# Optimization experiments

Hardware: AMD Instinct MI355X
Metric: run time of the kernel (lower is better)

## Reference

```python
import jax, jax.numpy as jnp
import numpy as np

N_NODES = 100000
N_EDGES = 400000
N_GRAPHS = 5000
IN, H, OUT = 11, 256, 1


def setup_inputs() -> dict:
    key = jax.random.key(0)
    ks = jax.random.split(key, 16)

    def xav(k, shape):
        fan_in, fan_out = shape[-2], shape[-1]
        std = float(np.sqrt(2.0 / (fan_in + fan_out)))
        return jax.random.normal(k, shape, dtype=jnp.float32) * std

    x = jax.random.normal(ks[0], (N_NODES, IN), dtype=jnp.float32)
    edge_index = jax.random.randint(ks[1], (2, N_EDGES), 0, N_NODES, dtype=jnp.int64)
    batch = jnp.sort(jax.random.randint(ks[2], (N_NODES,), 0, N_GRAPHS, dtype=jnp.int64))
    return {
        "x": x,
        "edge_index": edge_index,
        "batch": batch,
        "gin0_w1": xav(ks[3], (IN, H)),
        "gin0_b1": jnp.zeros((H,), jnp.float32),
        "gin0_w2": xav(ks[4], (H, H)),
        "gin0_b2": jnp.zeros((H,), jnp.float32),
        "gin_w1": xav(ks[5], (4, H, H)),
        "gin_b1": jnp.zeros((4, H), jnp.float32),
        "gin_w2": xav(ks[6], (4, H, H)),
        "gin_b2": jnp.zeros((4, H), jnp.float32),
        "head_w1": xav(ks[7], (H, H)),
        "head_b1": jnp.zeros((H,), jnp.float32),
        "head_w2": xav(ks[8], (H, OUT)),
        "head_b2": jnp.zeros((OUT,), jnp.float32),
    }


def _gin(x, src, dst, w1, b1, w2, b2):
    # GINConv (eps=0): MLP(x + sum_{j->i} x_j), then outer ReLU from forward()
    agg = jax.ops.segment_sum(x[src], dst, num_segments=N_NODES)
    h = x + agg
    h = jnp.matmul(jax.nn.relu(jnp.matmul(h, w1) + b1), w2) + b2
    return jax.nn.relu(h)  # dropout p=0.15 is identity in eval


def reference(x, edge_index, batch, gin0_w1, gin0_b1, gin0_w2, gin0_b2,
              gin_w1, gin_b1, gin_w2, gin_b2,
              head_w1, head_b1, head_w2, head_b2):
    src, dst = edge_index[0], edge_index[1]
    h = _gin(x, src, dst, gin0_w1, gin0_b1, gin0_w2, gin0_b2)
    for i in range(4):
        h = _gin(h, src, dst, gin_w1[i], gin_b1[i], gin_w2[i], gin_b2[i])
    # global mean pool over graphs
    sums = jax.ops.segment_sum(h, batch, num_segments=N_GRAPHS)
    cnts = jax.ops.segment_sum(jnp.ones((h.shape[0],), h.dtype), batch, num_segments=N_GRAPHS)
    pooled = sums / jnp.maximum(cnts, 1.0)[:, None]
    # head: Linear -> Dropout(0.25, identity in eval) -> Linear
    out = jnp.matmul(pooled, head_w1) + head_b1
    out = jnp.matmul(out, head_w2) + head_b2
    return out
```

## Files before the change

### kernel.cpp

```cpp
#include <hip/hip_runtime.h>
#include <hip/hip_bf16.h>


constexpr int HDIM = 256;

typedef short v8s __attribute__((ext_vector_type(8)));
typedef float v4f __attribute__((ext_vector_type(4)));

__device__ __forceinline__ float bflo(unsigned int u) { return __uint_as_float(u << 16); }
__device__ __forceinline__ float bfhi(unsigned int u) { return __uint_as_float(u & 0xffff0000u); }
__device__ __forceinline__ unsigned short f2bf(float f) {
    unsigned int u = __float_as_uint(f);
    return (unsigned short)((u + 0x7fffu + ((u >> 16) & 1u)) >> 16);
}

__device__ __forceinline__ void gload16(const void* g, void* l) {
    __builtin_amdgcn_global_load_lds(
        (const __attribute__((address_space(1))) unsigned int*)g,
        (__attribute__((address_space(3))) unsigned int*)l, 16, 0, 0);
}

__global__ __launch_bounds__(256) void hist_kernel(
    const int* __restrict__ dst, int* __restrict__ deg, int n_edges)
{
    int e = blockIdx.x * 256 + threadIdx.x;
    if (e < n_edges) atomicAdd(&deg[dst[e]], 1);
}

__global__ __launch_bounds__(256) void scan1_kernel(
    const int* __restrict__ deg, int* __restrict__ scanex,
    int* __restrict__ partials, int n)
{
    __shared__ int s[256];
    int i = blockIdx.x * 256 + threadIdx.x;
    int v = (i < n) ? deg[i] : 0;
    s[threadIdx.x] = v;
    __syncthreads();
#pragma unroll
    for (int off = 1; off < 256; off <<= 1) {
        int t = (threadIdx.x >= off) ? s[threadIdx.x - off] : 0;
        __syncthreads();
        s[threadIdx.x] += t;
        __syncthreads();
    }
    if (i < n) scanex[i] = s[threadIdx.x] - v;
    if (threadIdx.x == 255) partials[blockIdx.x] = s[255];
}

__global__ __launch_bounds__(512) void scan2_kernel(int* __restrict__ partials, int nb)
{
    __shared__ int s[512];
    int v = (threadIdx.x < nb) ? partials[threadIdx.x] : 0;
    s[threadIdx.x] = v;
    __syncthreads();
#pragma unroll
    for (int off = 1; off < 512; off <<= 1) {
        int t = (threadIdx.x >= off) ? s[threadIdx.x - off] : 0;
        __syncthreads();
        s[threadIdx.x] += t;
        __syncthreads();
    }
    if (threadIdx.x < nb) partials[threadIdx.x] = s[threadIdx.x] - v;
}

__global__ __launch_bounds__(256) void scan3_kernel(
    const int* __restrict__ scanex, const int* __restrict__ partials,
    int* __restrict__ rowptr, int* __restrict__ cursor, int n, int n_edges)
{
    int i = blockIdx.x * 256 + threadIdx.x;
    if (i < n) {
        int v = scanex[i] + partials[blockIdx.x];
        rowptr[i] = v;
        cursor[i] = v;
    }
    if (i == 0) rowptr[n] = n_edges;
}

__global__ __launch_bounds__(256) void fill_kernel(
    const int* __restrict__ src, const int* __restrict__ dst,
    int* __restrict__ cursor, int* __restrict__ csr_src, int n_edges)
{
    int e = blockIdx.x * 256 + threadIdx.x;
    if (e >= n_edges) return;
    int slot = atomicAdd(&cursor[dst[e]], 1);
    csr_src[slot] = src[e];
}

__global__ __launch_bounds__(256) void convw_kernel(
    const float* __restrict__ g0w2, const float* __restrict__ gw1,
    const float* __restrict__ gw2, unsigned short* __restrict__ Bts)
{
    int gid = blockIdx.x * 256 + threadIdx.x;
    if (gid >= 9 * 65536) return;
    int m = gid >> 16;
    int e = gid & 0xffff;
    int n = e >> 8, k = e & 255;
    const float* W = (m == 0) ? g0w2
                   : (m <= 4) ? gw1 + (size_t)(m - 1) * 65536
                              : gw2 + (size_t)(m - 5) * 65536;
    Bts[(size_t)m * 65536 + n * 256 + k] = f2bf(W[k * 256 + n]);
}

__global__ __launch_bounds__(256) void agg0_kernel(
    const float* __restrict__ x, const int* __restrict__ rowptr,
    const int* __restrict__ csr_src, float* __restrict__ xsum, int n)
{
    int gid = blockIdx.x * 256 + threadIdx.x;
    int node = gid >> 4, f = gid & 15;
    if (node >= n || f >= 11) return;
    float acc = x[(size_t)node * 11 + f];
    int beg = rowptr[node], end = rowptr[node + 1];
    for (int e = beg; e < end; e++)
        acc += x[(size_t)csr_src[e] * 11 + f];
    xsum[(size_t)node * 11 + f] = acc;
}

__global__ __launch_bounds__(256) void agg_bf_kernel(
    const unsigned short* __restrict__ h, const int* __restrict__ rowptr,
    const int* __restrict__ csr_src, unsigned short* __restrict__ out, int n)
{
    int node = blockIdx.x * 8 + (threadIdx.x >> 5);
    if (node >= n) return;
    int l = threadIdx.x & 31;
    uint4 raw = *(const uint4*)&h[(size_t)node * HDIM + l * 8];
    float a0 = bflo(raw.x), a1 = bfhi(raw.x), a2 = bflo(raw.y), a3 = bfhi(raw.y);
    float a4 = bflo(raw.z), a5 = bfhi(raw.z), a6 = bflo(raw.w), a7 = bfhi(raw.w);
    int beg = rowptr[node], end = rowptr[node + 1];
    for (int e = beg; e < end; e++) {
        int s = csr_src[e];
        uint4 r = *(const uint4*)&h[(size_t)s * HDIM + l * 8];
        a0 += bflo(r.x); a1 += bfhi(r.x); a2 += bflo(r.y); a3 += bfhi(r.y);
        a4 += bflo(r.z); a5 += bfhi(r.z); a6 += bflo(r.w); a7 += bfhi(r.w);
    }
    uint4 o;
    o.x = (unsigned int)f2bf(a0) | ((unsigned int)f2bf(a1) << 16);
    o.y = (unsigned int)f2bf(a2) | ((unsigned int)f2bf(a3) << 16);
    o.z = (unsigned int)f2bf(a4) | ((unsigned int)f2bf(a5) << 16);
    o.w = (unsigned int)f2bf(a6) | ((unsigned int)f2bf(a7) << 16);
    *(uint4*)&out[(size_t)node * HDIM + l * 8] = o;
}

__global__ __launch_bounds__(256) void gemm0_kernel(
    const float* __restrict__ xsum, const float* __restrict__ w1,
    const float* __restrict__ b1, unsigned short* __restrict__ out, int M)
{
    int row = blockIdx.x * 4 + (threadIdx.x >> 6);
    if (row >= M) return;
    int lane = threadIdx.x & 63;
    float xr[11];
#pragma unroll
    for (int k = 0; k < 11; k++) xr[k] = xsum[(size_t)row * 11 + k];
    int n = lane * 4;
    float4 acc = *(const float4*)&b1[n];
#pragma unroll
    for (int k = 0; k < 11; k++) {
        float4 w = *(const float4*)&w1[k * HDIM + n];
        acc.x = fmaf(xr[k], w.x, acc.x);
        acc.y = fmaf(xr[k], w.y, acc.y);
        acc.z = fmaf(xr[k], w.z, acc.z);
        acc.w = fmaf(xr[k], w.w, acc.w);
    }
    uint2 o;
    o.x = (unsigned int)f2bf(fmaxf(acc.x, 0.f)) | ((unsigned int)f2bf(fmaxf(acc.y, 0.f)) << 16);
    o.y = (unsigned int)f2bf(fmaxf(acc.z, 0.f)) | ((unsigned int)f2bf(fmaxf(acc.w, 0.f)) << 16);
    *(uint2*)&out[(size_t)row * HDIM + n] = o;
}

__global__ __launch_bounds__(256) void gemm_mfma(
    const unsigned short* __restrict__ A, const unsigned short* __restrict__ Wt,
    const float* __restrict__ bias, unsigned short* __restrict__ C,
    int M, int do_relu)
{
    __shared__ short lds[2][512 * 8];
    const int tid = threadIdx.x;
    const int w = tid >> 6, lane = tid & 63;
    const int q = lane >> 4, r = lane & 15;
    const int rh = w & 1, ch = w >> 1;
    const int m0 = blockIdx.x * 128, n0 = blockIdx.y * 128;

    v4f acc[4][4];
#pragma unroll
    for (int i = 0; i < 4; i++)
#pragma unroll
        for (int j = 0; j < 4; j++)
            acc[i][j] = (v4f){0.f, 0.f, 0.f, 0.f};

    for (int kt = 0; kt < HDIM; kt += 32) {
#pragma unroll
        for (int rd = 0; rd < 2; rd++) {
            int cb = rd * 256 + w * 64;
            int s  = cb + lane;
            int row = s >> 2;
            int ko  = ((s & 3) - (row >> 1)) & 3;
            int gr = m0 + row; if (gr >= M) gr = M - 1;
            gload16(&A[(size_t)gr * HDIM + kt + ko * 8],  &lds[0][cb * 8]);
            gload16(&Wt[(size_t)(n0 + row) * HDIM + kt + ko * 8], &lds[1][cb * 8]);
        }
        __syncthreads();
        v8s af[4], bf[4];
#pragma unroll
        for (int mi = 0; mi < 4; mi++) {
            int row = rh * 64 + mi * 16 + r;
            int slot = row * 4 + ((q + (row >> 1)) & 3);
            af[mi] = *(const v8s*)&lds[0][slot * 8];
        }
#pragma unroll
        for (int ni = 0; ni < 4; ni++) {
            int row = ch * 64 + ni * 16 + r;
            int slot = row * 4 + ((q + (row >> 1)) & 3);
            bf[ni] = *(const v8s*)&lds[1][slot * 8];
        }
#pragma unroll
        for (int mi = 0; mi < 4; mi++)
#pragma unroll
            for (int ni = 0; ni < 4; ni++)
                acc[mi][ni] = __builtin_amdgcn_mfma_f32_16x16x32_bf16(
                    af[mi], bf[ni], acc[mi][ni], 0, 0, 0);
        __syncthreads();
    }

    float bv[4];
#pragma unroll
    for (int ni = 0; ni < 4; ni++)
        bv[ni] = bias[n0 + ch * 64 + ni * 16 + r];

    short* cw = &lds[0][0] + w * (16 * 72);
#pragma unroll
    for (int mi = 0; mi < 4; mi++) {
#pragma unroll
        for (int ni = 0; ni < 4; ni++)
#pragma unroll
            for (int i = 0; i < 4; i++) {
                float v = acc[mi][ni][i] + bv[ni];
                if (do_relu) v = fmaxf(v, 0.f);
                cw[(q * 4 + i) * 72 + ni * 16 + r] = (short)f2bf(v);
            }
        __syncthreads();
        int row = lane >> 2, seg = lane & 3;
        int gm = m0 + rh * 64 + mi * 16 + row;
        if (gm < M) {
            v8s p0 = *(const v8s*)&cw[row * 72 + seg * 16];
            v8s p1 = *(const v8s*)&cw[row * 72 + seg * 16 + 8];
            size_t o = (size_t)gm * HDIM + n0 + ch * 64 + seg * 16;
            *(v8s*)&C[o]     = p0;
            *(v8s*)&C[o + 8] = p1;
        }
        __syncthreads();
    }
}

__global__ __launch_bounds__(256) void mlp_fused(
    const unsigned short* __restrict__ A,
    const unsigned short* __restrict__ W1t, const float* __restrict__ b1,
    const unsigned short* __restrict__ W2t, const float* __restrict__ b2,
    unsigned short* __restrict__ C, int M)
{
    __shared__ short Ybuf[8 * 2048];
    __shared__ short Astage[256 * 8];
    __shared__ short Wstage[1024 * 8];
    const int tid = threadIdx.x;
    const int w = tid >> 6, lane = tid & 63;
    const int q = lane >> 4, r = lane & 15;
    const int m0 = blockIdx.x * 64;

    v4f acc[4][4];
#pragma unroll
    for (int i = 0; i < 4; i++)
#pragma unroll
        for (int j = 0; j < 4; j++)
            acc[i][j] = (v4f){0.f, 0.f, 0.f, 0.f};

    for (int kc = 0; kc < 8; kc++) {
        int kt = kc * 32;
        {
            int s = tid;
            int row = s >> 2;
            int ko = ((s & 3) - (row >> 1)) & 3;
            int gr = m0 + row; if (gr >= M) gr = M - 1;
            gload16(&A[(size_t)gr * HDIM + kt + ko * 8], &Astage[(w * 64) * 8]);
        }
#pragma unroll
        for (int rd = 0; rd < 4; rd++) {
            int cb = rd * 256 + w * 64;
            int s = cb + lane;
            int n = s >> 2;
            int ko = ((s & 3) - (n >> 1)) & 3;
            gload16(&W1t[(size_t)n * HDIM + kt + ko * 8], &Wstage[cb * 8]);
        }
        __syncthreads();
        v8s af[4], bf[4];
#pragma unroll
        for (int mi = 0; mi < 4; mi++) {
            int row = mi * 16 + r;
            int slot = row * 4 + ((q + (row >> 1)) & 3);
            af[mi] = *(const v8s*)&Astage[slot * 8];
        }
#pragma unroll
        for (int ni = 0; ni < 4; ni++) {
            int n = w * 64 + ni * 16 + r;
            int slot = n * 4 + ((q + (n >> 1)) & 3);
            bf[ni] = *(const v8s*)&Wstage[slot * 8];
        }
#pragma unroll
        for (int mi = 0; mi < 4; mi++)
#pragma unroll
            for (int ni = 0; ni < 4; ni++)
                acc[mi][ni] = __builtin_amdgcn_mfma_f32_16x16x32_bf16(
                    af[mi], bf[ni], acc[mi][ni], 0, 0, 0);
        __syncthreads();
    }

    {
        float bv1[4];
#pragma unroll
        for (int ni = 0; ni < 4; ni++)
            bv1[ni] = b1[w * 64 + ni * 16 + r];
#pragma unroll
        for (int mi = 0; mi < 4; mi++)
#pragma unroll
            for (int ni = 0; ni < 4; ni++)
#pragma unroll
                for (int i = 0; i < 4; i++) {
                    float v = fmaxf(acc[mi][ni][i] + bv1[ni], 0.f);
                    int row = mi * 16 + q * 4 + i;
                    int col = w * 64 + ni * 16 + r;
                    int chunk = col >> 5, kk = col & 31;
                    int ko = kk >> 3, j = kk & 7;
                    int slot = row * 4 + ((ko + (row >> 1)) & 3);
                    Ybuf[chunk * 2048 + slot * 8 + j] = (short)f2bf(v);
                }
    }
    __syncthreads();

    v4f acc2[4][4];
#pragma unroll
    for (int i = 0; i < 4; i++)
#pragma unroll
        for (int j = 0; j < 4; j++)
            acc2[i][j] = (v4f){0.f, 0.f, 0.f, 0.f};

    for (int kc = 0; kc < 8; kc++) {
        int kt = kc * 32;
#pragma unroll
        for (int rd = 0; rd < 4; rd++) {
            int cb = rd * 256 + w * 64;
            int s = cb + lane;
            int n = s >> 2;
            int ko = ((s & 3) - (n >> 1)) & 3;
            gload16(&W2t[(size_t)n * HDIM + kt + ko * 8], &Wstage[cb * 8]);
        }
        __syncthreads();
        v8s af[4], bf[4];
#pragma unroll
        for (int mi = 0; mi < 4; mi++) {
            int row = mi * 16 + r;
            int slot = row * 4 + ((q + (row >> 1)) & 3);
            af[mi] = *(const v8s*)&Ybuf[kc * 2048 + slot * 8];
        }
#pragma unroll
        for (int ni = 0; ni < 4; ni++) {
            int n = w * 64 + ni * 16 + r;
            int slot = n * 4 + ((q + (n >> 1)) & 3);
            bf[ni] = *(const v8s*)&Wstage[slot * 8];
        }
#pragma unroll
        for (int mi = 0; mi < 4; mi++)
#pragma unroll
            for (int ni = 0; ni < 4; ni++)
                acc2[mi][ni] = __builtin_amdgcn_mfma_f32_16x16x32_bf16(
                    af[mi], bf[ni], acc2[mi][ni], 0, 0, 0);
        __syncthreads();
    }

    float bv2[4];
#pragma unroll
    for (int ni = 0; ni < 4; ni++)
        bv2[ni] = b2[w * 64 + ni * 16 + r];
    short* cw = &Ybuf[w * 1152];
#pragma unroll
    for (int mi = 0; mi < 4; mi++) {
#pragma unroll
        for (int ni = 0; ni < 4; ni++)
#pragma unroll
            for (int i = 0; i < 4; i++) {
                float v = fmaxf(acc2[mi][ni][i] + bv2[ni], 0.f);
                cw[(q * 4 + i) * 72 + ni * 16 + r] = (short)f2bf(v);
            }
        __syncthreads();
        int row = lane >> 2, seg = lane & 3;
        int gm = m0 + mi * 16 + row;
        if (gm < M) {
            v8s p0 = *(const v8s*)&cw[row * 72 + seg * 16];
            v8s p1 = *(const v8s*)&cw[row * 72 + seg * 16 + 8];
            size_t o = (size_t)gm * HDIM + w * 64 + seg * 16;
            *(v8s*)&C[o]     = p0;
            *(v8s*)&C[o + 8] = p1;
        }
        __syncthreads();
    }
}

__global__ __launch_bounds__(256) void gemm_head(
    const float* __restrict__ A, const float* __restrict__ B,
    const float* __restrict__ bias, float* __restrict__ C, int M)
{
    __shared__ float As[16][132];
    __shared__ float Bs[16][132];
    const int tid = threadIdx.x;
    const int tx = tid & 15, ty = tid >> 4;
    const int m0 = blockIdx.x * 128, n0 = blockIdx.y * 128;
    const int arow = tid >> 1, acs = (tid & 1) * 8;
    int gr = m0 + arow; if (gr >= M) gr = M - 1;
    float acc[8][8] = {};

    for (int kt = 0; kt < HDIM; kt += 16) {
        float f[8];
        *(float4*)&f[0] = *(const float4*)&A[(size_t)gr * HDIM + kt + acs];
        *(float4*)&f[4] = *(const float4*)&A[(size_t)gr * HDIM + kt + acs + 4];
#pragma unroll
        for (int j = 0; j < 8; j++) As[acs + j][arow] = f[j];
#pragma unroll
        for (int i = 0; i < 2; i++) {
            int lid = tid * 2 + i;
            int kr = lid >> 5, ns = (lid & 31) * 4;
            *(float4*)&Bs[kr][ns] =
                *(const float4*)&B[(size_t)(kt + kr) * HDIM + n0 + ns];
        }
        __syncthreads();
#pragma unroll
        for (int kl = 0; kl < 16; kl++) {
            float a[8], b[8];
            *(float4*)&a[0] = *(const float4*)&As[kl][ty * 8];
            *(float4*)&a[4] = *(const float4*)&As[kl][ty * 8 + 4];
            *(float4*)&b[0] = *(const float4*)&Bs[kl][tx * 8];
            *(float4*)&b[4] = *(const float4*)&Bs[kl][tx * 8 + 4];
#pragma unroll
            for (int i = 0; i < 8; i++)
#pragma unroll
                for (int j = 0; j < 8; j++)
                    acc[i][j] = fmaf(a[i], b[j], acc[i][j]);
        }
        __syncthreads();
    }

    float bv[8];
    *(float4*)&bv[0] = *(const float4*)&bias[n0 + tx * 8];
    *(float4*)&bv[4] = *(const float4*)&bias[n0 + tx * 8 + 4];
#pragma unroll
    for (int i = 0; i < 8; i++) {
        int gr2 = m0 + ty * 8 + i;
        if (gr2 >= M) break;
        float o[8];
#pragma unroll
        for (int j = 0; j < 8; j++) o[j] = acc[i][j] + bv[j];
        *(float4*)&C[(size_t)gr2 * HDIM + n0 + tx * 8]     = *(float4*)&o[0];
        *(float4*)&C[(size_t)gr2 * HDIM + n0 + tx * 8 + 4] = *(float4*)&o[4];
    }
}

__global__ __launch_bounds__(256) void bounds_kernel(
    const int* __restrict__ batch, int* __restrict__ gstart, int n, int ngraphs)
{
    int i = blockIdx.x * 256 + threadIdx.x;
    if (i >= n) return;
    int b1 = batch[i];
    int b0 = (i == 0) ? -1 : batch[i - 1];
    for (int g = b0 + 1; g <= b1; g++) gstart[g] = i;
    if (i == n - 1)
        for (int g = b1 + 1; g <= ngraphs; g++) gstart[g] = n;
}

__global__ __launch_bounds__(256) void pool_kernel(
    const unsigned short* __restrict__ h, const int* __restrict__ gstart,
    float* __restrict__ pooled, int ngraphs)
{
    int g = blockIdx.x * 4 + (threadIdx.x >> 6);
    if (g >= ngraphs) return;
    int lane = threadIdx.x & 63;
    int beg = gstart[g], end = gstart[g + 1];
    float a0 = 0.f, a1 = 0.f, a2 = 0.f, a3 = 0.f;
    for (int i = beg; i < end; i++) {
        uint2 r = *(const uint2*)&h[(size_t)i * HDIM + lane * 4];
        a0 += bflo(r.x); a1 += bfhi(r.x); a2 += bflo(r.y); a3 += bfhi(r.y);
    }
    float inv = 1.0f / fmaxf((float)(end - beg), 1.0f);
    float4 o = { a0 * inv, a1 * inv, a2 * inv, a3 * inv };
    *(float4*)&pooled[(size_t)g * HDIM + lane * 4] = o;
}

__global__ __launch_bounds__(256) void head2_kernel(
    const float* __restrict__ hh, const float* __restrict__ w2,
    const float* __restrict__ b2, float* __restrict__ out, int n_graphs)
{
    int g = blockIdx.x * 4 + (threadIdx.x >> 6);
    int lane = threadIdx.x & 63;
    float p = 0.f;
    if (g < n_graphs) {
        float4 v = *(const float4*)&hh[(size_t)g * HDIM + lane * 4];
        float4 w = *(const float4*)&w2[lane * 4];
        p = v.x * w.x + v.y * w.y + v.z * w.z + v.w * w.w;
    }
#pragma unroll
    for (int off = 32; off > 0; off >>= 1) p += __shfl_down(p, off, 64);
    if (g < n_graphs && lane == 0) out[g] = p + b2[0];
}

extern "C" void kernel_launch(void* const* d_in, const int* in_sizes, int n_in,
                              void* d_out, int out_size, void* d_ws, size_t ws_size,
                              hipStream_t stream)
{
    const float* x    = (const float*)d_in[0];
    const int*   ei   = (const int*)d_in[1];
    const int*   batch= (const int*)d_in[2];
    const float* g0w1 = (const float*)d_in[3];
    const float* g0b1 = (const float*)d_in[4];
    const float* g0w2 = (const float*)d_in[5];
    const float* g0b2 = (const float*)d_in[6];
    const float* gw1  = (const float*)d_in[7];
    const float* gb1  = (const float*)d_in[8];
    const float* gw2  = (const float*)d_in[9];
    const float* gb2  = (const float*)d_in[10];
    const float* hw1  = (const float*)d_in[11];
    const float* hb1  = (const float*)d_in[12];
    const float* hw2  = (const float*)d_in[13];
    const float* hb2  = (const float*)d_in[14];

    const int n_nodes  = in_sizes[0] / 11;
    const int n_edges  = in_sizes[1] / 2;
    const int n_graphs = out_size;

    const int* srcp = ei;
    const int* dstp = ei + n_edges;

    const size_t NF = (size_t)n_nodes * HDIM;
    char* p = (char*)d_ws;
    unsigned short* H0 = (unsigned short*)p; p += NF * 2;
    unsigned short* H1 = (unsigned short*)p; p += NF * 2;
    unsigned short* Bts = (unsigned short*)p; p += (size_t)9 * 65536 * 2;
    float* xsum    = (float*)p; p += (size_t)n_nodes * 11 * 4;
    float* pooled  = (float*)p; p += (size_t)n_graphs * HDIM * 4;
    float* hh      = (float*)p; p += (size_t)n_graphs * HDIM * 4;
    int* deg       = (int*)p; p += (size_t)n_nodes * 4;
    int* scanex    = (int*)p; p += (size_t)n_nodes * 4;
    int* partials  = (int*)p; p += 512 * 4;
    int* rowptr    = (int*)p; p += ((size_t)n_nodes + 1) * 4;
    int* cursor    = (int*)p; p += (size_t)n_nodes * 4;
    int* csr_src   = (int*)p; p += (size_t)n_edges * 4;
    int* gstart    = (int*)p; p += ((size_t)n_graphs + 1) * 4;
    if ((size_t)(p - (char*)d_ws) > ws_size) return;

    const int nblk = (n_nodes + 255) / 256;

    convw_kernel<<<(9 * 65536 + 255) / 256, 256, 0, stream>>>(g0w2, gw1, gw2, Bts);

    hipMemsetAsync(deg, 0, (size_t)n_nodes * 4, stream);
    hist_kernel<<<(n_edges + 255) / 256, 256, 0, stream>>>(dstp, deg, n_edges);
    scan1_kernel<<<nblk, 256, 0, stream>>>(deg, scanex, partials, n_nodes);
    scan2_kernel<<<1, 512, 0, stream>>>(partials, nblk);
    scan3_kernel<<<nblk, 256, 0, stream>>>(scanex, partials, rowptr, cursor,
                                           n_nodes, n_edges);
    fill_kernel<<<(n_edges + 255) / 256, 256, 0, stream>>>(
        srcp, dstp, cursor, csr_src, n_edges);

    bounds_kernel<<<nblk, 256, 0, stream>>>(batch, gstart, n_nodes, n_graphs);

    agg0_kernel<<<((size_t)n_nodes * 16 + 255) / 256, 256, 0, stream>>>(
        x, rowptr, csr_src, xsum, n_nodes);
    gemm0_kernel<<<(n_nodes + 3) / 4, 256, 0, stream>>>(xsum, g0w1, g0b1, H1, n_nodes);
    gemm_mfma<<<dim3((n_nodes + 127) / 128, 2), 256, 0, stream>>>(
        H1, Bts + 0, g0b2, H0, n_nodes, 1);

    unsigned short* cur = H0;
    unsigned short* t   = H1;
    const int aggGrid = (n_nodes + 7) / 8;
    const int mlpGrid = (n_nodes + 63) / 64;
    for (int l = 0; l < 4; l++) {
        agg_bf_kernel<<<aggGrid, 256, 0, stream>>>(cur, rowptr, csr_src, t, n_nodes);
        mlp_fused<<<mlpGrid, 256, 0, stream>>>(
            t, Bts + (size_t)(1 + l) * 65536, gb1 + (size_t)l * HDIM,
            Bts + (size_t)(5 + l) * 65536, gb2 + (size_t)l * HDIM,
            cur, n_nodes);
    }

    pool_kernel<<<(n_graphs + 3) / 4, 256, 0, stream>>>(cur, gstart, pooled, n_graphs);

    gemm_head<<<dim3((n_graphs + 127) / 128, 2), 256, 0, stream>>>(
        pooled, hw1, hb1, hh, n_graphs);
    head2_kernel<<<(n_graphs + 3) / 4, 256, 0, stream>>>(
        hh, hw2, hb2, (float*)d_out, n_graphs);
}
```

Before: 665.2 us.

## Keep GEMM weight fragments in registers and load activations directly from global

The layer GEMMs (gemm_reg and fused MLP) now preload each wave's 64-column slice of the weight matrix into registers once, instead of staging weights and activations through LDS every K step. Activation fragments are read straight from global memory, which removes the per-iteration barriers. The epilogue uses double-buffered per-wave LDS staging so it needs fewer syncs. The edge aggregation loop is unrolled by two to keep more gathers in flight. This costs a large register footprint (128 VGPRs of weights plus 64 accumulators) under a 2-blocks-per-CU launch bound, so there is spill or occupancy risk, and the global A loads are uncoalesced 16-byte row fragments.

```diff
diff --git a/kernel.cpp b/kernel.cpp
--- a/kernel.cpp
+++ b/kernel.cpp
@@ -12,12 +12,6 @@
 __device__ __forceinline__ unsigned short f2bf(float f) {
     unsigned int u = __float_as_uint(f);
     return (unsigned short)((u + 0x7fffu + ((u >> 16) & 1u)) >> 16);
-}
-
-__device__ __forceinline__ void gload16(const void* g, void* l) {
-    __builtin_amdgcn_global_load_lds(
-        (const __attribute__((address_space(1))) unsigned int*)g,
-        (__attribute__((address_space(3))) unsigned int*)l, 16, 0, 0);
 }
 
 __global__ __launch_bounds__(256) void hist_kernel(
@@ -126,11 +120,21 @@
     float a0 = bflo(raw.x), a1 = bfhi(raw.x), a2 = bflo(raw.y), a3 = bfhi(raw.y);
     float a4 = bflo(raw.z), a5 = bfhi(raw.z), a6 = bflo(raw.w), a7 = bfhi(raw.w);
     int beg = rowptr[node], end = rowptr[node + 1];
-    for (int e = beg; e < end; e++) {
-        int s = csr_src[e];
-        uint4 r = *(const uint4*)&h[(size_t)s * HDIM + l * 8];
-        a0 += bflo(r.x); a1 += bfhi(r.x); a2 += bflo(r.y); a3 += bfhi(r.y);
-        a4 += bflo(r.z); a5 += bfhi(r.z); a6 += bflo(r.w); a7 += bfhi(r.w);
+    int e = beg;
+    for (; e + 1 < end; e += 2) {
+        int s0 = csr_src[e], s1 = csr_src[e + 1];
+        uint4 r0 = *(const uint4*)&h[(size_t)s0 * HDIM + l * 8];
+        uint4 r1 = *(const uint4*)&h[(size_t)s1 * HDIM + l * 8];
+        a0 += bflo(r0.x); a1 += bfhi(r0.x); a2 += bflo(r0.y); a3 += bfhi(r0.y);
+        a4 += bflo(r0.z); a5 += bfhi(r0.z); a6 += bflo(r0.w); a7 += bfhi(r0.w);
+        a0 += bflo(r1.x); a1 += bfhi(r1.x); a2 += bflo(r1.y); a3 += bfhi(r1.y);
+        a4 += bflo(r1.z); a5 += bfhi(r1.z); a6 += bflo(r1.w); a7 += bfhi(r1.w);
+    }
+    if (e < end) {
+        int s0 = csr_src[e];
+        uint4 r0 = *(const uint4*)&h[(size_t)s0 * HDIM + l * 8];
+        a0 += bflo(r0.x); a1 += bfhi(r0.x); a2 += bflo(r0.y); a3 += bfhi(r0.y);
+        a4 += bflo(r0.z); a5 += bfhi(r0.z); a6 += bflo(r0.w); a7 += bfhi(r0.w);
     }
     uint4 o;
     o.x = (unsigned int)f2bf(a0) | ((unsigned int)f2bf(a1) << 16);
@@ -166,17 +170,23 @@
     *(uint2*)&out[(size_t)row * HDIM + n] = o;
 }
 
-__global__ __launch_bounds__(256) void gemm_mfma(
+__global__ __launch_bounds__(256, 2) void gemm_reg(
     const unsigned short* __restrict__ A, const unsigned short* __restrict__ Wt,
     const float* __restrict__ bias, unsigned short* __restrict__ C,
     int M, int do_relu)
 {
-    __shared__ short lds[2][512 * 8];
+    __shared__ short ebuf[4 * 2304];
     const int tid = threadIdx.x;
     const int w = tid >> 6, lane = tid & 63;
     const int q = lane >> 4, r = lane & 15;
-    const int rh = w & 1, ch = w >> 1;
-    const int m0 = blockIdx.x * 128, n0 = blockIdx.y * 128;
+    const int m0 = blockIdx.x * 64;
+
+    v8s wf[8][4];
+#pragma unroll
+    for (int kc = 0; kc < 8; kc++)
+#pragma unroll
+        for (int ni = 0; ni < 4; ni++)
+            wf[kc][ni] = *(const v8s*)&Wt[(size_t)(w * 64 + ni * 16 + r) * HDIM + kc * 32 + q * 8];
 
     v4f acc[4][4];
 #pragma unroll
@@ -185,48 +195,29 @@
         for (int j = 0; j < 4; j++)
             acc[i][j] = (v4f){0.f, 0.f, 0.f, 0.f};
 
-    for (int kt = 0; kt < HDIM; kt += 32) {
-#pragma unroll
-        for (int rd = 0; rd < 2; rd++) {
-            int cb = rd * 256 + w * 64;
-            int s  = cb + lane;
-            int row = s >> 2;
-            int ko  = ((s & 3) - (row >> 1)) & 3;
-            int gr = m0 + row; if (gr >= M) gr = M - 1;
-            gload16(&A[(size_t)gr * HDIM + kt + ko * 8],  &lds[0][cb * 8]);
-            gload16(&Wt[(size_t)(n0 + row) * HDIM + kt + ko * 8], &lds[1][cb * 8]);
-        }
-        __syncthreads();
-        v8s af[4], bf[4];
+#pragma unroll
+    for (int kc = 0; kc < 8; kc++) {
+        v8s af[4];
 #pragma unroll
         for (int mi = 0; mi < 4; mi++) {
-            int row = rh * 64 + mi * 16 + r;
-            int slot = row * 4 + ((q + (row >> 1)) & 3);
-            af[mi] = *(const v8s*)&lds[0][slot * 8];
-        }
-#pragma unroll
-        for (int ni = 0; ni < 4; ni++) {
-            int row = ch * 64 + ni * 16 + r;
-            int slot = row * 4 + ((q + (row >> 1)) & 3);
-            bf[ni] = *(const v8s*)&lds[1][slot * 8];
+            int gr = m0 + mi * 16 + r; if (gr >= M) gr = M - 1;
+            af[mi] = *(const v8s*)&A[(size_t)gr * HDIM + kc * 32 + q * 8];
         }
 #pragma unroll
         for (int mi = 0; mi < 4; mi++)
 #pragma unroll
             for (int ni = 0; ni < 4; ni++)
                 acc[mi][ni] = __builtin_amdgcn_mfma_f32_16x16x32_bf16(
-                    af[mi], bf[ni], acc[mi][ni], 0, 0, 0);
-        __syncthreads();
+                    af[mi], wf[kc][ni], acc[mi][ni], 0, 0, 0);
     }
 
     float bv[4];
 #pragma unroll
     for (int ni = 0; ni < 4; ni++)
-        bv[ni] = bias[n0 + ch * 64 + ni * 16 + r];
-
-    short* cw = &lds[0][0] + w * (16 * 72);
+        bv[ni] = bias[w * 64 + ni * 16 + r];
 #pragma unroll
     for (int mi = 0; mi < 4; mi++) {
+        short* cw = &ebuf[w * 2304 + (mi & 1) * 1152];
 #pragma unroll
         for (int ni = 0; ni < 4; ni++)
 #pragma unroll
@@ -235,34 +226,37 @@
                 if (do_relu) v = fmaxf(v, 0.f);
                 cw[(q * 4 + i) * 72 + ni * 16 + r] = (short)f2bf(v);
             }
-        __syncthreads();
         int row = lane >> 2, seg = lane & 3;
-        int gm = m0 + rh * 64 + mi * 16 + row;
+        int gm = m0 + mi * 16 + row;
         if (gm < M) {
             v8s p0 = *(const v8s*)&cw[row * 72 + seg * 16];
             v8s p1 = *(const v8s*)&cw[row * 72 + seg * 16 + 8];
-            size_t o = (size_t)gm * HDIM + n0 + ch * 64 + seg * 16;
+            size_t o = (size_t)gm * HDIM + w * 64 + seg * 16;
             *(v8s*)&C[o]     = p0;
             *(v8s*)&C[o + 8] = p1;
         }
-        __syncthreads();
-    }
-}
-
-__global__ __launch_bounds__(256) void mlp_fused(
+    }
+}
+
+__global__ __launch_bounds__(256, 2) void mlp_fused(
     const unsigned short* __restrict__ A,
     const unsigned short* __restrict__ W1t, const float* __restrict__ b1,
     const unsigned short* __restrict__ W2t, const float* __restrict__ b2,
     unsigned short* __restrict__ C, int M)
 {
     __shared__ short Ybuf[8 * 2048];
-    __shared__ short Astage[256 * 8];
-    __shared__ short Wstage[1024 * 8];
     const int tid = threadIdx.x;
     const int w = tid >> 6, lane = tid & 63;
     const int q = lane >> 4, r = lane & 15;
     const int m0 = blockIdx.x * 64;
 
+    v8s wf[8][4];
+#pragma unroll
+    for (int kc = 0; kc < 8; kc++)
+#pragma unroll
+        for (int ni = 0; ni < 4; ni++)
+            wf[kc][ni] = *(const v8s*)&W1t[(size_t)(w * 64 + ni * 16 + r) * HDIM + kc * 32 + q * 8];
+
     v4f acc[4][4];
 #pragma unroll
     for (int i = 0; i < 4; i++)
@@ -270,44 +264,20 @@
         for (int j = 0; j < 4; j++)
             acc[i][j] = (v4f){0.f, 0.f, 0.f, 0.f};
 
+#pragma unroll
     for (int kc = 0; kc < 8; kc++) {
-        int kt = kc * 32;
-        {
-            int s = tid;
-            int row = s >> 2;
-            int ko = ((s & 3) - (row >> 1)) & 3;
-            int gr = m0 + row; if (gr >= M) gr = M - 1;
-            gload16(&A[(size_t)gr * HDIM + kt + ko * 8], &Astage[(w * 64) * 8]);
-        }
-#pragma unroll
-        for (int rd = 0; rd < 4; rd++) {
-            int cb = rd * 256 + w * 64;
-            int s = cb + lane;
-            int n = s >> 2;
-            int ko = ((s & 3) - (n >> 1)) & 3;
-            gload16(&W1t[(size_t)n * HDIM + kt + ko * 8], &Wstage[cb * 8]);
-        }
-        __syncthreads();
-        v8s af[4], bf[4];
+        v8s af[4];
 #pragma unroll
         for (int mi = 0; mi < 4; mi++) {
-            int row = mi * 16 + r;
-            int slot = row * 4 + ((q + (row >> 1)) & 3);
-            af[mi] = *(const v8s*)&Astage[slot * 8];
-        }
-#pragma unroll
-        for (int ni = 0; ni < 4; ni++) {
-            int n = w * 64 + ni * 16 + r;
-            int slot = n * 4 + ((q + (n >> 1)) & 3);
-            bf[ni] = *(const v8s*)&Wstage[slot * 8];
+            int gr = m0 + mi * 16 + r; if (gr >= M) gr = M - 1;
+            af[mi] = *(const v8s*)&A[(size_t)gr * HDIM + kc * 32 + q * 8];
         }
 #pragma unroll
         for (int mi = 0; mi < 4; mi++)
 #pragma unroll
             for (int ni = 0; ni < 4; ni++)
                 acc[mi][ni] = __builtin_amdgcn_mfma_f32_16x16x32_bf16(
-                    af[mi], bf[ni], acc[mi][ni], 0, 0, 0);
-        __syncthreads();
+                    af[mi], wf[kc][ni], acc[mi][ni], 0, 0, 0);
     }
 
     {
@@ -332,25 +302,21 @@
     }
     __syncthreads();
 
-    v4f acc2[4][4];
+#pragma unroll
+    for (int kc = 0; kc < 8; kc++)
+#pragma unroll
+        for (int ni = 0; ni < 4; ni++)
+            wf[kc][ni] = *(const v8s*)&W2t[(size_t)(w * 64 + ni * 16 + r) * HDIM + kc * 32 + q * 8];
+
 #pragma unroll
     for (int i = 0; i < 4; i++)
 #pragma unroll
         for (int j = 0; j < 4; j++)
-            acc2[i][j] = (v4f){0.f, 0.f, 0.f, 0.f};
-
+            acc[i][j] = (v4f){0.f, 0.f, 0.f, 0.f};
+
+#pragma unroll
     for (int kc = 0; kc < 8; kc++) {
-        int kt = kc * 32;
-#pragma unroll
-        for (int rd = 0; rd < 4; rd++) {
-            int cb = rd * 256 + w * 64;
-            int s = cb + lane;
-            int n = s >> 2;
-            int ko = ((s & 3) - (n >> 1)) & 3;
-            gload16(&W2t[(size_t)n * HDIM + kt + ko * 8], &Wstage[cb * 8]);
-        }
-        __syncthreads();
-        v8s af[4], bf[4];
+        v8s af[4];
 #pragma unroll
         for (int mi = 0; mi < 4; mi++) {
             int row = mi * 16 + r;
@@ -358,35 +324,28 @@
             af[mi] = *(const v8s*)&Ybuf[kc * 2048 + slot * 8];
         }
 #pragma unroll
-        for (int ni = 0; ni < 4; ni++) {
-            int n = w * 64 + ni * 16 + r;
-            int slot = n * 4 + ((q + (n >> 1)) & 3);
-            bf[ni] = *(const v8s*)&Wstage[slot * 8];
-        }
-#pragma unroll
         for (int mi = 0; mi < 4; mi++)
 #pragma unroll
             for (int ni = 0; ni < 4; ni++)
-                acc2[mi][ni] = __builtin_amdgcn_mfma_f32_16x16x32_bf16(
-                    af[mi], bf[ni], acc2[mi][ni], 0, 0, 0);
-        __syncthreads();
-    }
+                acc[mi][ni] = __builtin_amdgcn_mfma_f32_16x16x32_bf16(
+                    af[mi], wf[kc][ni], acc[mi][ni], 0, 0, 0);
+    }
+    __syncthreads();
 
     float bv2[4];
 #pragma unroll
     for (int ni = 0; ni < 4; ni++)
         bv2[ni] = b2[w * 64 + ni * 16 + r];
-    short* cw = &Ybuf[w * 1152];
 #pragma unroll
     for (int mi = 0; mi < 4; mi++) {
+        short* cw = &Ybuf[w * 2304 + (mi & 1) * 1152];
 #pragma unroll
         for (int ni = 0; ni < 4; ni++)
 #pragma unroll
             for (int i = 0; i < 4; i++) {
-                float v = fmaxf(acc2[mi][ni][i] + bv2[ni], 0.f);
+                float v = fmaxf(acc[mi][ni][i] + bv2[ni], 0.f);
                 cw[(q * 4 + i) * 72 + ni * 16 + r] = (short)f2bf(v);
             }
-        __syncthreads();
         int row = lane >> 2, seg = lane & 3;
         int gm = m0 + mi * 16 + row;
         if (gm < M) {
@@ -396,7 +355,6 @@
             *(v8s*)&C[o]     = p0;
             *(v8s*)&C[o + 8] = p1;
         }
-        __syncthreads();
     }
 }
 
@@ -564,19 +522,19 @@
 
     bounds_kernel<<<nblk, 256, 0, stream>>>(batch, gstart, n_nodes, n_graphs);
 
+    const int tileGrid = (n_nodes + 63) / 64;
+
     agg0_kernel<<<((size_t)n_nodes * 16 + 255) / 256, 256, 0, stream>>>(
         x, rowptr, csr_src, xsum, n_nodes);
     gemm0_kernel<<<(n_nodes + 3) / 4, 256, 0, stream>>>(xsum, g0w1, g0b1, H1, n_nodes);
-    gemm_mfma<<<dim3((n_nodes + 127) / 128, 2), 256, 0, stream>>>(
-        H1, Bts + 0, g0b2, H0, n_nodes, 1);
+    gemm_reg<<<tileGrid, 256, 0, stream>>>(H1, Bts + 0, g0b2, H0, n_nodes, 1);
 
     unsigned short* cur = H0;
     unsigned short* t   = H1;
     const int aggGrid = (n_nodes + 7) / 8;
-    const int mlpGrid = (n_nodes + 63) / 64;
     for (int l = 0; l < 4; l++) {
         agg_bf_kernel<<<aggGrid, 256, 0, stream>>>(cur, rowptr, csr_src, t, n_nodes);
-        mlp_fused<<<mlpGrid, 256, 0, stream>>>(
+        mlp_fused<<<tileGrid, 256, 0, stream>>>(
             t, Bts + (size_t)(1 + l) * 65536, gb1 + (size_t)l * HDIM,
             Bts + (size_t)(5 + l) * 65536, gb2 + (size_t)l * HDIM,
             cur, n_nodes);
```

New measurement: 832.9 us. 1.25x slower.

## Fuse neighbor aggregation into the GIN MLP kernel via shared-memory staging

Applied to the files above, without the earlier changes.

Merges the per-layer aggregation kernel into the fused MLP kernel. Each 64-row tile gathers and sums its neighbor rows directly into a swizzled LDS buffer that serves as the GEMM A operand, and that buffer is then reused for the hidden activations. This removes one launch per layer and the bf16 round trip of the aggregated features through global memory, and it ping-pongs the output buffers so a layer never overwrites its own input. It also unrolls the edge loop by two, sets a minimum-occupancy launch bound, and drops the epilogue barriers by giving each wave double-buffered staging space. The trade-off is that the irregular gather latency now sits inside the GEMM kernel and is not overlapped with other work, and occupancy is limited by register and LDS use.

```diff
diff --git a/kernel.cpp b/kernel.cpp
--- a/kernel.cpp
+++ b/kernel.cpp
@@ -115,31 +115,6 @@
     xsum[(size_t)node * 11 + f] = acc;
 }
 
-__global__ __launch_bounds__(256) void agg_bf_kernel(
-    const unsigned short* __restrict__ h, const int* __restrict__ rowptr,
-    const int* __restrict__ csr_src, unsigned short* __restrict__ out, int n)
-{
-    int node = blockIdx.x * 8 + (threadIdx.x >> 5);
-    if (node >= n) return;
-    int l = threadIdx.x & 31;
-    uint4 raw = *(const uint4*)&h[(size_t)node * HDIM + l * 8];
-    float a0 = bflo(raw.x), a1 = bfhi(raw.x), a2 = bflo(raw.y), a3 = bfhi(raw.y);
-    float a4 = bflo(raw.z), a5 = bfhi(raw.z), a6 = bflo(raw.w), a7 = bfhi(raw.w);
-    int beg = rowptr[node], end = rowptr[node + 1];
-    for (int e = beg; e < end; e++) {
-        int s = csr_src[e];
-        uint4 r = *(const uint4*)&h[(size_t)s * HDIM + l * 8];
-        a0 += bflo(r.x); a1 += bfhi(r.x); a2 += bflo(r.y); a3 += bfhi(r.y);
-        a4 += bflo(r.z); a5 += bfhi(r.z); a6 += bflo(r.w); a7 += bfhi(r.w);
-    }
-    uint4 o;
-    o.x = (unsigned int)f2bf(a0) | ((unsigned int)f2bf(a1) << 16);
-    o.y = (unsigned int)f2bf(a2) | ((unsigned int)f2bf(a3) << 16);
-    o.z = (unsigned int)f2bf(a4) | ((unsigned int)f2bf(a5) << 16);
-    o.w = (unsigned int)f2bf(a6) | ((unsigned int)f2bf(a7) << 16);
-    *(uint4*)&out[(size_t)node * HDIM + l * 8] = o;
-}
-
 __global__ __launch_bounds__(256) void gemm0_kernel(
     const float* __restrict__ xsum, const float* __restrict__ w1,
     const float* __restrict__ b1, unsigned short* __restrict__ out, int M)
@@ -249,19 +224,52 @@
     }
 }
 
-__global__ __launch_bounds__(256) void mlp_fused(
-    const unsigned short* __restrict__ A,
+__global__ __launch_bounds__(256, 3) void gin_layer(
+    const unsigned short* __restrict__ h,
+    const int* __restrict__ rowptr, const int* __restrict__ csr_src,
     const unsigned short* __restrict__ W1t, const float* __restrict__ b1,
     const unsigned short* __restrict__ W2t, const float* __restrict__ b2,
     unsigned short* __restrict__ C, int M)
 {
-    __shared__ short Ybuf[8 * 2048];
-    __shared__ short Astage[256 * 8];
-    __shared__ short Wstage[1024 * 8];
+    __shared__ short AY[16384];
+    __shared__ short Wstage[8192];
     const int tid = threadIdx.x;
     const int w = tid >> 6, lane = tid & 63;
     const int q = lane >> 4, r = lane & 15;
+    const int hw = tid >> 5, l = tid & 31;
     const int m0 = blockIdx.x * 64;
+
+    for (int it = 0; it < 8; it++) {
+        int row = it * 8 + hw;
+        int node = m0 + row; if (node >= M) node = M - 1;
+        uint4 raw = *(const uint4*)&h[(size_t)node * HDIM + l * 8];
+        float a0 = bflo(raw.x), a1 = bfhi(raw.x), a2 = bflo(raw.y), a3 = bfhi(raw.y);
+        float a4 = bflo(raw.z), a5 = bfhi(raw.z), a6 = bflo(raw.w), a7 = bfhi(raw.w);
+        int beg = rowptr[node], end = rowptr[node + 1];
+        int e = beg;
+        for (; e + 1 < end; e += 2) {
+            int s0 = csr_src[e], s1 = csr_src[e + 1];
+            uint4 r0 = *(const uint4*)&h[(size_t)s0 * HDIM + l * 8];
+            uint4 r1 = *(const uint4*)&h[(size_t)s1 * HDIM + l * 8];
+            a0 += bflo(r0.x); a1 += bfhi(r0.x); a2 += bflo(r0.y); a3 += bfhi(r0.y);
+            a4 += bflo(r0.z); a5 += bfhi(r0.z); a6 += bflo(r0.w); a7 += bfhi(r0.w);
+            a0 += bflo(r1.x); a1 += bfhi(r1.x); a2 += bflo(r1.y); a3 += bfhi(r1.y);
+            a4 += bflo(r1.z); a5 += bfhi(r1.z); a6 += bflo(r1.w); a7 += bfhi(r1.w);
+        }
+        if (e < end) {
+            int s0 = csr_src[e];
+            uint4 r0 = *(const uint4*)&h[(size_t)s0 * HDIM + l * 8];
+            a0 += bflo(r0.x); a1 += bfhi(r0.x); a2 += bflo(r0.y); a3 += bfhi(r0.y);
+            a4 += bflo(r0.z); a5 += bfhi(r0.z); a6 += bflo(r0.w); a7 += bfhi(r0.w);
+        }
+        uint4 o;
+        o.x = (unsigned int)f2bf(a0) | ((unsigned int)f2bf(a1) << 16);
+        o.y = (unsigned int)f2bf(a2) | ((unsigned int)f2bf(a3) << 16);
+        o.z = (unsigned int)f2bf(a4) | ((unsigned int)f2bf(a5) << 16);
+        o.w = (unsigned int)f2bf(a6) | ((unsigned int)f2bf(a7) << 16);
+        int slot = row * 4 + (((l & 3) + (row >> 1)) & 3);
+        *(uint4*)&AY[(l >> 2) * 2048 + slot * 8] = o;
+    }
 
     v4f acc[4][4];
 #pragma unroll
@@ -271,21 +279,13 @@
             acc[i][j] = (v4f){0.f, 0.f, 0.f, 0.f};
 
     for (int kc = 0; kc < 8; kc++) {
-        int kt = kc * 32;
-        {
-            int s = tid;
-            int row = s >> 2;
-            int ko = ((s & 3) - (row >> 1)) & 3;
-            int gr = m0 + row; if (gr >= M) gr = M - 1;
-            gload16(&A[(size_t)gr * HDIM + kt + ko * 8], &Astage[(w * 64) * 8]);
-        }
 #pragma unroll
         for (int rd = 0; rd < 4; rd++) {
             int cb = rd * 256 + w * 64;
             int s = cb + lane;
             int n = s >> 2;
             int ko = ((s & 3) - (n >> 1)) & 3;
-            gload16(&W1t[(size_t)n * HDIM + kt + ko * 8], &Wstage[cb * 8]);
+            gload16(&W1t[(size_t)n * HDIM + kc * 32 + ko * 8], &Wstage[cb * 8]);
         }
         __syncthreads();
         v8s af[4], bf[4];
@@ -293,7 +293,7 @@
         for (int mi = 0; mi < 4; mi++) {
             int row = mi * 16 + r;
             int slot = row * 4 + ((q + (row >> 1)) & 3);
-            af[mi] = *(const v8s*)&Astage[slot * 8];
+            af[mi] = *(const v8s*)&AY[kc * 2048 + slot * 8];
         }
 #pragma unroll
         for (int ni = 0; ni < 4; ni++) {
@@ -327,7 +327,7 @@
                     int chunk = col >> 5, kk = col & 31;
                     int ko = kk >> 3, j = kk & 7;
                     int slot = row * 4 + ((ko + (row >> 1)) & 3);
-                    Ybuf[chunk * 2048 + slot * 8 + j] = (short)f2bf(v);
+                    AY[chunk * 2048 + slot * 8 + j] = (short)f2bf(v);
                 }
     }
     __syncthreads();
@@ -340,14 +340,13 @@
             acc2[i][j] = (v4f){0.f, 0.f, 0.f, 0.f};
 
     for (int kc = 0; kc < 8; kc++) {
-        int kt = kc * 32;
 #pragma unroll
         for (int rd = 0; rd < 4; rd++) {
             int cb = rd * 256 + w * 64;
             int s = cb + lane;
             int n = s >> 2;
             int ko = ((s & 3) - (n >> 1)) & 3;
-            gload16(&W2t[(size_t)n * HDIM + kt + ko * 8], &Wstage[cb * 8]);
+            gload16(&W2t[(size_t)n * HDIM + kc * 32 + ko * 8], &Wstage[cb * 8]);
         }
         __syncthreads();
         v8s af[4], bf[4];
@@ -355,7 +354,7 @@
         for (int mi = 0; mi < 4; mi++) {
             int row = mi * 16 + r;
             int slot = row * 4 + ((q + (row >> 1)) & 3);
-            af[mi] = *(const v8s*)&Ybuf[kc * 2048 + slot * 8];
+            af[mi] = *(const v8s*)&AY[kc * 2048 + slot * 8];
         }
 #pragma unroll
         for (int ni = 0; ni < 4; ni++) {
@@ -376,9 +375,9 @@
 #pragma unroll
     for (int ni = 0; ni < 4; ni++)
         bv2[ni] = b2[w * 64 + ni * 16 + r];
-    short* cw = &Ybuf[w * 1152];
 #pragma unroll
     for (int mi = 0; mi < 4; mi++) {
+        short* cw = &AY[w * 2304 + (mi & 1) * 1152];
 #pragma unroll
         for (int ni = 0; ni < 4; ni++)
 #pragma unroll
@@ -386,7 +385,6 @@
                 float v = fmaxf(acc2[mi][ni][i] + bv2[ni], 0.f);
                 cw[(q * 4 + i) * 72 + ni * 16 + r] = (short)f2bf(v);
             }
-        __syncthreads();
         int row = lane >> 2, seg = lane & 3;
         int gm = m0 + mi * 16 + row;
         if (gm < M) {
@@ -396,7 +394,6 @@
             *(v8s*)&C[o]     = p0;
             *(v8s*)&C[o + 8] = p1;
         }
-        __syncthreads();
     }
 }
 
@@ -570,16 +567,16 @@
     gemm_mfma<<<dim3((n_nodes + 127) / 128, 2), 256, 0, stream>>>(
         H1, Bts + 0, g0b2, H0, n_nodes, 1);
 
+    const int tileGrid = (n_nodes + 63) / 64;
     unsigned short* cur = H0;
-    unsigned short* t   = H1;
-    const int aggGrid = (n_nodes + 7) / 8;
-    const int mlpGrid = (n_nodes + 63) / 64;
+    unsigned short* oth = H1;
     for (int l = 0; l < 4; l++) {
-        agg_bf_kernel<<<aggGrid, 256, 0, stream>>>(cur, rowptr, csr_src, t, n_nodes);
-        mlp_fused<<<mlpGrid, 256, 0, stream>>>(
-            t, Bts + (size_t)(1 + l) * 65536, gb1 + (size_t)l * HDIM,
+        gin_layer<<<tileGrid, 256, 0, stream>>>(
+            cur, rowptr, csr_src,
+            Bts + (size_t)(1 + l) * 65536, gb1 + (size_t)l * HDIM,
             Bts + (size_t)(5 + l) * 65536, gb2 + (size_t)l * HDIM,
-            cur, n_nodes);
+            oth, n_nodes);
+        unsigned short* t = cur; cur = oth; oth = t;
     }
 
     pool_kernel<<<(n_graphs + 3) / 4, 256, 0, stream>>>(cur, gstart, pooled, n_graphs);
```

After: 704.4 us. 5.9% more time.
